# Kernel optimization log

Hardware: AMD Instinct MI355X
Metric: run time of the kernel (lower is better)

## Reference

```python
import jax, jax.numpy as jnp
import numpy as np

B = 65536
N_HOSTS = 16
N_FEATS = 48        # 3 * n_hosts
N_WINDOW = 3
N_LATENT = 10
GAT_IN = 3
GAT_OUT = 16
E = N_WINDOW + GAT_OUT  # 19, MHA embed dim
PROTO_DIM = 10


def setup_inputs() -> dict:
    key = jax.random.key(0)
    ks = jax.random.split(key, 20)
    def rn(k, shape, scale=0.1):
        return jax.random.normal(k, shape, dtype=jnp.float32) * scale
    return {
        "t": jax.random.normal(ks[0], (B, N_WINDOW, N_FEATS), dtype=jnp.float32),
        "s": jnp.zeros((1,), jnp.float32),  # unused by forward, kept for signature fidelity
        "h0": jax.random.normal(ks[1], (B, 1, N_WINDOW), dtype=jnp.float32),
        "gru_Wih": rn(ks[2], (3 * N_WINDOW, N_FEATS)),
        "gru_Whh": rn(ks[3], (3 * N_WINDOW, N_WINDOW)),
        "gru_bih": rn(ks[4], (3 * N_WINDOW,)),
        "gru_bhh": rn(ks[5], (3 * N_WINDOW,)),
        "gat_W": rn(ks[6], (GAT_IN, GAT_OUT)),
        "gat_al": rn(ks[7], (GAT_OUT,)),
        "gat_ar": rn(ks[8], (GAT_OUT,)),
        "mha_Win": rn(ks[9], (3 * E, E)),
        "mha_bin": rn(ks[10], (3 * E,)),
        "mha_Wout": rn(ks[11], (E, E)),
        "mha_bout": rn(ks[12], (E,)),
        "enc_W": rn(ks[13], (N_HOSTS * N_LATENT, N_WINDOW * E)),
        "enc_b": rn(ks[14], (N_HOSTS * N_LATENT,)),
        "anom_W": rn(ks[15], (2, N_LATENT)),
        "anom_b": rn(ks[16], (2,)),
        "proto_W": rn(ks[17], (PROTO_DIM, N_LATENT)),
        "proto_b": rn(ks[18], (PROTO_DIM,)),
    }


def _forward(t, s, h0, gru_Wih, gru_Whh, gru_bih, gru_bhh,
             gat_W, gat_al, gat_ar, mha_Win, mha_bin, mha_Wout, mha_bout,
             enc_W, enc_b, anom_W, anom_b, proto_W, proto_b):
    # ---- GRU (seq-first, batch B, hidden = n_window = 3) ----
    xs = jnp.swapaxes(t, 0, 1)  # (3, B, 48)
    h0_ = h0[:, 0, :]           # (B, 3)

    def gru_step(h, x_t):
        gi = x_t @ gru_Wih.T + gru_bih   # (B, 9)
        gh = h @ gru_Whh.T + gru_bhh     # (B, 9)
        i_r, i_z, i_n = jnp.split(gi, 3, axis=-1)
        h_r, h_z, h_n = jnp.split(gh, 3, axis=-1)
        r = jax.nn.sigmoid(i_r + h_r)
        z = jax.nn.sigmoid(i_z + h_z)
        n = jnp.tanh(i_n + r * h_n)
        h_new = (1.0 - z) * n + z * h
        return h_new, h_new

    _, gru_out = jax.lax.scan(gru_step, h0_, xs)  # (3, B, 3)

    # ---- GAT on fully-connected 16-node graph (with self loops) ----
    gin = t.reshape(t.shape[0], N_WINDOW, N_HOSTS, GAT_IN)      # (B, 3, 16, 3)
    z = jnp.einsum("bwnc,cf->bwnf", gin, gat_W)                 # (B, 3, 16, 16)
    el = z @ gat_al                                              # src scores (B,3,16)
    er = z @ gat_ar                                              # dst scores (B,3,16)
    e = jax.nn.leaky_relu(er[..., :, None] + el[..., None, :], 0.2)  # (B,3,v,u)
    alpha = jax.nn.softmax(e, axis=-1)                           # softmax over sources u
    gat_nodes = jnp.einsum("bwvu,bwuf->bwvf", alpha, z)          # (B, 3, 16, 16)
    gat_out = gat_nodes.mean(axis=2)                             # (B, 3, 16) mean over hosts
    gat_out = jnp.swapaxes(gat_out, 0, 1)                        # (3, B, 16)

    # ---- concat + single-head MHA (embed=19) ----
    c = jnp.concatenate([gru_out, gat_out], axis=-1)             # (3, B, 19)
    Wq, Wk, Wv = jnp.split(mha_Win, 3, axis=0)
    bq, bk, bv = jnp.split(mha_bin, 3, axis=0)
    q = c @ Wq.T + bq
    k = c @ Wk.T + bk
    v = c @ Wv.T + bv
    scores = jnp.einsum("sbe,tbe->bst", q, k) / jnp.sqrt(jnp.float32(E))
    attw = jax.nn.softmax(scores, axis=-1)
    attn = jnp.einsum("bst,tbe->sbe", attw, v)
    attn = attn @ mha_Wout.T + mha_bout                          # (3, B, 19)

    # ---- encoder: Linear(57,160); LeakyReLU(True) => negative_slope=1.0 => identity ----
    flat = jnp.swapaxes(attn, 0, 1).reshape(-1, N_WINDOW * E)    # (B, 57), seq-major flatten
    latent = flat @ enc_W.T + enc_b                              # (B, 160)
    latent = latent.reshape(-1, N_HOSTS, N_LATENT)               # (B, 16, 10)

    # ---- per-host tiny decoders, vectorized ----
    anomaly = jax.nn.softmax(latent @ anom_W.T + anom_b, axis=-1)   # (B, 16, 2)
    proto = jax.nn.sigmoid(latent @ proto_W.T + proto_b)            # (B, 16, PROTO_DIM)
    return anomaly, proto


def reference(t, s, h0, gru_Wih, gru_Whh, gru_bih, gru_bhh,
              gat_W, gat_al, gat_ar, mha_Win, mha_bin, mha_Wout, mha_bout,
              enc_W, enc_b, anom_W, anom_b, proto_W, proto_b):
    return _forward(t, s, h0, gru_Wih, gru_Whh, gru_bih, gru_bhh,
                    gat_W, gat_al, gat_ar, mha_Win, mha_bin, mha_Wout, mha_bout,
                    enc_W, enc_b, anom_W, anom_b, proto_W, proto_b)
```

## Files before the change

kernel.cpp:

```cpp
#include <hip/hip_runtime.h>

#define NW 3
#define NF 48
#define NHOST 16
#define NLAT 10
#define GOUT 16
#define EDIM 19
#define PDIM 10

#define CB_M    0
#define CB_P    361
#define CB_G    722
#define CB_H    741
#define CB_R    760
#define CB_C0   779
#define CB_WAL  780
#define CB_WAR  783
#define CB_CBIG 800
#define CB_BF   976
#define CB_TOT  10240

typedef __attribute__((ext_vector_type(8))) short bf16x8;
typedef __attribute__((ext_vector_type(4))) float f32x4;

__device__ __forceinline__ float frcp(float x){ return __builtin_amdgcn_rcpf(x); }
__device__ __forceinline__ float fsig(float x){ return frcp(1.f + __expf(-x)); }
__device__ __forceinline__ float ftanh(float x){ return 1.f - 2.f*frcp(1.f + __expf(2.f*x)); }
__device__ __forceinline__ unsigned short f2bf(float x){
    union { float f; unsigned u; } v; v.f = x;
    unsigned r = v.u + 0x7FFFu + ((v.u >> 16) & 1u);
    return (unsigned short)(r >> 16);
}

__global__ __launch_bounds__(256) void k_const(
    const float* __restrict__ Win, const float* __restrict__ bin,
    const float* __restrict__ Wout, const float* __restrict__ bout,
    const float* __restrict__ gatW, const float* __restrict__ gal,
    const float* __restrict__ gar, const float* __restrict__ encW,
    const float* __restrict__ encb,
    const float* __restrict__ aW, const float* __restrict__ ab,
    const float* __restrict__ pW, const float* __restrict__ pb,
    float* __restrict__ cb)
{
    const int w = blockIdx.x*blockDim.x + threadIdx.x;
    if (w < 786) {
        const int idx = w;
        float acc = 0.f;
        if (idx < 361) {
            int i = idx/19, j = idx%19;
            for (int e = 0; e < EDIM; ++e) acc += Win[e*EDIM+i]*Win[(EDIM+e)*EDIM+j];
        } else if (idx < 722) {
            int k = idx-361; int i = k/19, j = k%19;
            for (int e = 0; e < EDIM; ++e) acc += Wout[i*EDIM+e]*Win[(2*EDIM+e)*EDIM+j];
        } else if (idx < 741) {
            int j = idx-722;
            for (int e = 0; e < EDIM; ++e) acc += bin[e]*Win[(EDIM+e)*EDIM+j];
        } else if (idx < 760) {
            int i = idx-741;
            for (int e = 0; e < EDIM; ++e) acc += Win[e*EDIM+i]*bin[EDIM+e];
        } else if (idx < 779) {
            int i = idx-760; acc = bout[i];
            for (int e = 0; e < EDIM; ++e) acc += Wout[i*EDIM+e]*bin[2*EDIM+e];
        } else if (idx == 779) {
            for (int e = 0; e < EDIM; ++e) acc += bin[e]*bin[EDIM+e];
        } else {
            int c = idx-780; int cc = c%3; bool left = c<3;
            for (int f2 = 0; f2 < GOUT; ++f2)
                acc += gatW[cc*GOUT+f2]*(left ? gal[f2] : gar[f2]);
        }
        cb[idx] = acc;
    } else if (w < 962) {
        const int g = w - 786;
        int host = g / 11, jj = g % 11;
        float acc = (jj == 0) ? (ab[0] - ab[1]) : pb[jj-1];
        for (int l = 0; l < NLAT; ++l) {
            float coef = (jj == 0) ? (aW[l] - aW[NLAT+l]) : pW[(jj-1)*NLAT + l];
            acc += coef * encb[host*NLAT + l];
        }
        cb[CB_CBIG + g] = acc;
    } else if (w < 12226) {
        unsigned short* bf = (unsigned short*)(cb + CB_BF);
        const int u = w - 962;
        int j    = u & 7;
        int lane = (u >> 3) & 63;
        int tile = u >> 9;
        int half = tile / 11, n = tile % 11;
        int k = half*32 + ((lane >> 4) & 3)*8 + j;
        int g = n*16 + (lane & 15);
        float acc = 0.f;
        if (k < 57) {
            int host = g / 11, jj = g % 11;
            for (int l = 0; l < NLAT; ++l) {
                float coef = (jj == 0) ? (aW[l] - aW[NLAT+l]) : pW[(jj-1)*NLAT + l];
                acc += coef * encW[(host*NLAT + l)*57 + k];
            }
        }
        bf[u] = f2bf(acc);
    }
}

__global__ __launch_bounds__(256) void k_fused(
    const float* __restrict__ t, const float* __restrict__ h0,
    const float* __restrict__ Wih, const float* __restrict__ bih,
    const float* __restrict__ gatW, const float* __restrict__ Whh,
    const float* __restrict__ bhh, const float* __restrict__ cb,
    float* __restrict__ outA, float* __restrict__ outP, int B)
{
    __shared__ __align__(16) char smraw[57344];
    __shared__ __align__(16) unsigned short a2[64][64];
    float (*fm)[25][64] = reinterpret_cast<float(*)[25][64]>(smraw);
    float* xs            = reinterpret_cast<float*>(smraw + 19200);
    float (*mtb)[EDIM][64] = reinterpret_cast<float(*)[EDIM][64]>(smraw + 19200);
    float (*gtb)[64]       = reinterpret_cast<float(*)[64]>(smraw + 19200 + 14592);
    float (*pcb)[EDIM][64] = reinterpret_cast<float(*)[EDIM][64]>(smraw + 19200 + 15360);
    float (*lg)[178]       = reinterpret_cast<float(*)[178]>(smraw);

    const int tid = threadIdx.x;
    const int b0  = blockIdx.x * 64;
    const int bl  = tid & 63;
    const int sw  = tid >> 6;

    if (tid < 192) {
        const int w = sw;
        const float* tp = t + ((size_t)(b0 + bl)*NW + w)*NF;
        float* xrow = xs + tid*49;

        const float Wal0=cb[CB_WAL],Wal1=cb[CB_WAL+1],Wal2=cb[CB_WAL+2];
        const float War0=cb[CB_WAR],War1=cb[CB_WAR+1],War2=cb[CB_WAR+2];

        float gi[9];
#pragma unroll
        for (int r = 0; r < 9; ++r) gi[r] = bih[r];
        float el[NHOST], er[NHOST];
#pragma unroll
        for (int c = 0; c < 4; ++c) {
            float xc[12];
#pragma unroll
            for (int i = 0; i < 3; ++i) {
                float4 v = *reinterpret_cast<const float4*>(tp + c*12 + i*4);
                xc[i*4+0]=v.x; xc[i*4+1]=v.y; xc[i*4+2]=v.z; xc[i*4+3]=v.w;
            }
#pragma unroll
            for (int k = 0; k < 12; ++k) xrow[c*12 + k] = xc[k];
#pragma unroll
            for (int r = 0; r < 9; ++r) {
                float a = 0.f;
#pragma unroll
                for (int k = 0; k < 12; ++k) a += xc[k]*Wih[r*NF + c*12 + k];
                gi[r] += a;
            }
#pragma unroll
            for (int u = 0; u < 4; ++u) {
                const int uu = c*4 + u;
                el[uu] = xc[u*3]*Wal0 + xc[u*3+1]*Wal1 + xc[u*3+2]*Wal2;
                er[uu] = xc[u*3]*War0 + xc[u*3+1]*War1 + xc[u*3+2]*War2;
            }
        }
#pragma unroll
        for (int r = 0; r < 9; ++r) fm[w][r][bl] = gi[r];

        float beta[NHOST];
#pragma unroll
        for (int u = 0; u < NHOST; ++u) beta[u] = 0.f;
#pragma unroll
        for (int v = 0; v < NHOST; ++v) {
            float ee[NHOST]; float sum = 0.f;
#pragma unroll
            for (int u = 0; u < NHOST; ++u) {
                float s = er[v] + el[u];
                s = fmaxf(s, 0.2f*s);
                ee[u] = __expf(s); sum += ee[u];
            }
            float inv = frcp(sum);
#pragma unroll
            for (int u = 0; u < NHOST; ++u) beta[u] += ee[u]*inv;
        }
        float g0=0.f, g1=0.f, g2=0.f;
#pragma unroll
        for (int u = 0; u < NHOST; ++u) {
            float bu = beta[u]*(1.f/16.f);
            g0 += bu*xrow[u*3+0]; g1 += bu*xrow[u*3+1]; g2 += bu*xrow[u*3+2];
        }
#pragma unroll
        for (int f2 = 0; f2 < GOUT; ++f2)
            fm[w][9+f2][bl] = g0*gatW[f2] + g1*gatW[GOUT+f2] + g2*gatW[2*GOUT+f2];
    }
    __syncthreads();

    float cw[EDIM];
    float hsv = 0.f, aw0 = 0.f, aw1 = 0.f, aw2 = 0.f;
#pragma unroll
    for (int i = 0; i < EDIM; ++i) cw[i] = 0.f;

    if (tid < 192) {
        const int s = sw;
        const int b = b0 + bl;
        float h[3] = { h0[(size_t)b*3+0], h0[(size_t)b*3+1], h0[(size_t)b*3+2] };
        float ch[NW][3];
#pragma unroll
        for (int w = 0; w < NW; ++w) {
            float gi[9];
#pragma unroll
            for (int r = 0; r < 9; ++r) gi[r] = fm[w][r][bl];
            float gh[9];
#pragma unroll
            for (int r = 0; r < 9; ++r)
                gh[r] = bhh[r] + h[0]*Whh[r*3+0] + h[1]*Whh[r*3+1] + h[2]*Whh[r*3+2];
#pragma unroll
            for (int j = 0; j < 3; ++j) {
                float rg = fsig(gi[j]   + gh[j]);
                float zg = fsig(gi[3+j] + gh[3+j]);
                float ng = ftanh(gi[6+j] + rg*gh[6+j]);
                h[j] = (1.f - zg)*ng + zg*h[j];
            }
            ch[w][0]=h[0]; ch[w][1]=h[1]; ch[w][2]=h[2];
        }
#pragma unroll
        for (int j = 0; j < 3; ++j)
            cw[j] = (s==0) ? ch[0][j] : (s==1) ? ch[1][j] : ch[2][j];
#pragma unroll
        for (int f2 = 0; f2 < GOUT; ++f2)
            cw[3+f2] = fm[s][9+f2][bl];

        float gt = 0.f;
#pragma unroll
        for (int i = 0; i < EDIM; ++i) { hsv += cw[i]*cb[CB_H+i]; gt += cw[i]*cb[CB_G+i]; }
#pragma unroll
        for (int i = 0; i < EDIM; ++i) {
            float a = 0.f;
#pragma unroll
            for (int j = 0; j < EDIM; ++j) a += cb[CB_M+i*EDIM+j]*cw[j];
            mtb[s][i][bl] = a;
        }
        gtb[s][bl] = gt;
    }
    __syncthreads();

    if (tid < 192) {
        const int s = sw;
        const float c0 = cb[CB_C0];
        float sc[NW];
#pragma unroll
        for (int tt = 0; tt < NW; ++tt) {
            float a = 0.f;
#pragma unroll
            for (int i = 0; i < EDIM; ++i) a += cw[i]*mtb[tt][i][bl];
            sc[tt] = (a + gtb[tt][bl] + hsv + c0) * 0.2294157338705618f;
        }
        float m = fmaxf(sc[0], fmaxf(sc[1], sc[2]));
        float e0=__expf(sc[0]-m), e1=__expf(sc[1]-m), e2=__expf(sc[2]-m);
        float inv = frcp(e0+e1+e2);
        aw0=e0*inv; aw1=e1*inv; aw2=e2*inv;

#pragma unroll
        for (int i = 0; i < EDIM; ++i) {
            float a = 0.f;
#pragma unroll
            for (int j = 0; j < EDIM; ++j) a += cb[CB_P+i*EDIM+j]*cw[j];
            pcb[s][i][bl] = a;
        }
    }
    __syncthreads();

    if (tid < 192) {
        const int s = sw;
        char* a2c = (char*)a2;
        const int swz = (bl & 7) << 4;
#pragma unroll
        for (int i = 0; i < EDIM; ++i) {
            float v = cb[CB_R+i] + aw0*pcb[0][i][bl] + aw1*pcb[1][i][bl]
                    + aw2*pcb[2][i][bl];
            const int byte = bl*128 + (s*EDIM + i)*2;
            *reinterpret_cast<unsigned short*>(a2c + (byte ^ swz)) = f2bf(v);
        }
        if (s == 0) {
#pragma unroll
            for (int r = 0; r < 7; ++r) {
                const int byte = bl*128 + (57 + r)*2;
                *reinterpret_cast<unsigned short*>(a2c + (byte ^ swz)) = 0;
            }
        }
    }
    __syncthreads();

    const int lane = tid & 63;
    const int wv   = __builtin_amdgcn_readfirstlane(sw);
    {
        const int browl = wv*16 + (lane & 15);
        const int koff  = (lane >> 4) * 8;
        const char* a2c = (const char*)a2;
        const int swz = (browl & 7) << 4;
        union { uint4 q; bf16x8 v; } a0, a1;
        a0.q = *reinterpret_cast<const uint4*>(a2c + ((browl*128 + koff*2) ^ swz));
        a1.q = *reinterpret_cast<const uint4*>(a2c + ((browl*128 + 64 + koff*2) ^ swz));

        const uint4* bfq = (const uint4*)(cb + CB_BF);
        const int r0 = wv*16 + ((lane >> 4) << 2);
#pragma unroll
        for (int n = 0; n < 11; ++n) {
            union { uint4 q; bf16x8 v; } bf0, bf1;
            bf0.q = bfq[(size_t)n*64 + lane];
            bf1.q = bfq[(size_t)(11 + n)*64 + lane];
            f32x4 acc = {0.f, 0.f, 0.f, 0.f};
            acc = __builtin_amdgcn_mfma_f32_16x16x32_bf16(a0.v, bf0.v, acc, 0, 0, 0);
            acc = __builtin_amdgcn_mfma_f32_16x16x32_bf16(a1.v, bf1.v, acc, 0, 0, 0);
            const int c = n*16 + (lane & 15);
#pragma unroll
            for (int r = 0; r < 4; ++r) lg[r0 + r][c] = acc[r];
        }
    }
    __syncthreads();

    {
        const int host = tid & 15;
        const int tg   = tid >> 4;
        const float* cbig = cb + CB_CBIG;
#pragma unroll
        for (int i = 0; i < 4; ++i) {
            const int bll = tg + 16*i;
            const int b   = b0 + bll;
            float v[11];
#pragma unroll
            for (int jj = 0; jj < 11; ++jj)
                v[jj] = lg[bll][host*11 + jj] + cbig[host*11 + jj];
            float p0 = fsig(v[0]);
            float2 av; av.x = p0; av.y = 1.f - p0;
            *reinterpret_cast<float2*>(outA + (size_t)b*32 + host*2) = av;
            float* pP = outP + (size_t)b*160 + host*10;
#pragma unroll
            for (int p = 0; p < 5; ++p) {
                float2 pv; pv.x = fsig(v[1 + 2*p]); pv.y = fsig(v[2 + 2*p]);
                *reinterpret_cast<float2*>(pP + 2*p) = pv;
            }
        }
    }
}

extern "C" void kernel_launch(void* const* d_in, const int* in_sizes, int n_in,
                              void* d_out, int out_size, void* d_ws, size_t ws_size,
                              hipStream_t stream) {
    const float* t    = (const float*)d_in[0];
    const float* h0   = (const float*)d_in[2];
    const float* Wih  = (const float*)d_in[3];
    const float* Whh  = (const float*)d_in[4];
    const float* bih  = (const float*)d_in[5];
    const float* bhh  = (const float*)d_in[6];
    const float* gatW = (const float*)d_in[7];
    const float* gal  = (const float*)d_in[8];
    const float* gar  = (const float*)d_in[9];
    const float* Win  = (const float*)d_in[10];
    const float* bin  = (const float*)d_in[11];
    const float* Wout = (const float*)d_in[12];
    const float* bout = (const float*)d_in[13];
    const float* encW = (const float*)d_in[14];
    const float* encb = (const float*)d_in[15];
    const float* aW   = (const float*)d_in[16];
    const float* ab   = (const float*)d_in[17];
    const float* pW   = (const float*)d_in[18];
    const float* pb   = (const float*)d_in[19];

    const int B = in_sizes[0] / (NW * NF);
    float* cb  = (float*)d_ws;
    float* outA = (float*)d_out;
    float* outP = (float*)d_out + (size_t)B*32;

    k_const<<<dim3(48), 256, 0, stream>>>(Win, bin, Wout, bout, gatW, gal, gar,
                                          encW, encb, aW, ab, pW, pb, cb);
    k_fused<<<dim3(B/64), 256, 0, stream>>>(t, h0, Wih, bih, gatW, Whh, bhh, cb,
                                            outA, outP, B);
}
```

Baseline: 64.97 us.

## Shrink fused kernel to single-wave blocks of 16 rows with compact LDS

Changes the fused kernel from 256-thread blocks over 64 batch rows to 64-thread single-wavefront blocks over 16 rows. It cuts LDS per block by storing the input rows as bf16 and the MFMA logits as fp16, and adds extra barriers so that aliased shared buffers are not overwritten early. The aim is higher occupancy and more blocks in flight, at the cost of 48 of 64 lanes working in the early stages, four times as many blocks, and lower precision in the intermediates.

Result: no change. 66.18 us (+1.9%).

```diff
diff --git a/kernel.cpp b/kernel.cpp
--- a/kernel.cpp
+++ b/kernel.cpp
@@ -30,6 +30,9 @@
     union { float f; unsigned u; } v; v.f = x;
     unsigned r = v.u + 0x7FFFu + ((v.u >> 16) & 1u);
     return (unsigned short)(r >> 16);
+}
+__device__ __forceinline__ float bf2f(unsigned short s){
+    union { unsigned u; float f; } v; v.u = ((unsigned)s) << 16; return v.f;
 }
 
 __global__ __launch_bounds__(256) void k_const(
@@ -99,31 +102,31 @@
     }
 }
 
-__global__ __launch_bounds__(256) void k_fused(
+__global__ __launch_bounds__(64, 4) void k_fused(
     const float* __restrict__ t, const float* __restrict__ h0,
     const float* __restrict__ Wih, const float* __restrict__ bih,
     const float* __restrict__ gatW, const float* __restrict__ Whh,
     const float* __restrict__ bhh, const float* __restrict__ cb,
     float* __restrict__ outA, float* __restrict__ outP, int B)
 {
-    __shared__ __align__(16) char smraw[57344];
-    __shared__ __align__(16) unsigned short a2[64][64];
-    float (*fm)[25][64] = reinterpret_cast<float(*)[25][64]>(smraw);
-    float* xs            = reinterpret_cast<float*>(smraw + 19200);
-    float (*mtb)[EDIM][64] = reinterpret_cast<float(*)[EDIM][64]>(smraw + 19200);
-    float (*gtb)[64]       = reinterpret_cast<float(*)[64]>(smraw + 19200 + 14592);
-    float (*pcb)[EDIM][64] = reinterpret_cast<float(*)[EDIM][64]>(smraw + 19200 + 15360);
-    float (*lg)[178]       = reinterpret_cast<float(*)[178]>(smraw);
-
-    const int tid = threadIdx.x;
-    const int b0  = blockIdx.x * 64;
-    const int bl  = tid & 63;
-    const int sw  = tid >> 6;
-
-    if (tid < 192) {
+    __shared__ __align__(16) char smraw[9600];
+    __shared__ __align__(16) unsigned short a2[16][64];
+    float (*fm)[25][16]     = reinterpret_cast<float(*)[25][16]>(smraw);
+    unsigned short (*xs)[50]= reinterpret_cast<unsigned short(*)[50]>(smraw + 4800);
+    float (*mtb)[EDIM][16]  = reinterpret_cast<float(*)[EDIM][16]>(smraw + 4800);
+    float (*pcb)[EDIM][16]  = reinterpret_cast<float(*)[EDIM][16]>(smraw + 4800);
+    float (*gtb)[16]        = reinterpret_cast<float(*)[16]>(smraw + 4800 + 3648);
+    _Float16 (*lg)[178]     = reinterpret_cast<_Float16(*)[178]>(smraw);
+
+    const int lane = threadIdx.x;
+    const int b0   = blockIdx.x * 16;
+    const int bl   = lane & 15;
+    const int sw   = lane >> 4;
+
+    if (lane < 48) {
         const int w = sw;
         const float* tp = t + ((size_t)(b0 + bl)*NW + w)*NF;
-        float* xrow = xs + tid*49;
+        unsigned short* xrow = xs[lane];
 
         const float Wal0=cb[CB_WAL],Wal1=cb[CB_WAL+1],Wal2=cb[CB_WAL+2];
         const float War0=cb[CB_WAR],War1=cb[CB_WAR+1],War2=cb[CB_WAR+2];
@@ -141,7 +144,7 @@
                 xc[i*4+0]=v.x; xc[i*4+1]=v.y; xc[i*4+2]=v.z; xc[i*4+3]=v.w;
             }
 #pragma unroll
-            for (int k = 0; k < 12; ++k) xrow[c*12 + k] = xc[k];
+            for (int k = 0; k < 12; ++k) xrow[c*12 + k] = f2bf(xc[k]);
 #pragma unroll
             for (int r = 0; r < 9; ++r) {
                 float a = 0.f;
@@ -179,7 +182,9 @@
 #pragma unroll
         for (int u = 0; u < NHOST; ++u) {
             float bu = beta[u]*(1.f/16.f);
-            g0 += bu*xrow[u*3+0]; g1 += bu*xrow[u*3+1]; g2 += bu*xrow[u*3+2];
+            g0 += bu*bf2f(xrow[u*3+0]);
+            g1 += bu*bf2f(xrow[u*3+1]);
+            g2 += bu*bf2f(xrow[u*3+2]);
         }
 #pragma unroll
         for (int f2 = 0; f2 < GOUT; ++f2)
@@ -192,7 +197,7 @@
 #pragma unroll
     for (int i = 0; i < EDIM; ++i) cw[i] = 0.f;
 
-    if (tid < 192) {
+    if (lane < 48) {
         const int s = sw;
         const int b = b0 + bl;
         float h[3] = { h0[(size_t)b*3+0], h0[(size_t)b*3+1], h0[(size_t)b*3+2] };
@@ -221,7 +226,11 @@
 #pragma unroll
         for (int f2 = 0; f2 < GOUT; ++f2)
             cw[3+f2] = fm[s][9+f2][bl];
-
+    }
+    __syncthreads();
+
+    if (lane < 48) {
+        const int s = sw;
         float gt = 0.f;
 #pragma unroll
         for (int i = 0; i < EDIM; ++i) { hsv += cw[i]*cb[CB_H+i]; gt += cw[i]*cb[CB_G+i]; }
@@ -236,8 +245,7 @@
     }
     __syncthreads();
 
-    if (tid < 192) {
-        const int s = sw;
+    if (lane < 48) {
         const float c0 = cb[CB_C0];
         float sc[NW];
 #pragma unroll
@@ -251,7 +259,11 @@
         float e0=__expf(sc[0]-m), e1=__expf(sc[1]-m), e2=__expf(sc[2]-m);
         float inv = frcp(e0+e1+e2);
         aw0=e0*inv; aw1=e1*inv; aw2=e2*inv;
-
+    }
+    __syncthreads();
+
+    if (lane < 48) {
+        const int s = sw;
 #pragma unroll
         for (int i = 0; i < EDIM; ++i) {
             float a = 0.f;
@@ -262,7 +274,7 @@
     }
     __syncthreads();
 
-    if (tid < 192) {
+    if (lane < 48) {
         const int s = sw;
         char* a2c = (char*)a2;
         const int swz = (bl & 7) << 4;
@@ -283,10 +295,8 @@
     }
     __syncthreads();
 
-    const int lane = tid & 63;
-    const int wv   = __builtin_amdgcn_readfirstlane(sw);
     {
-        const int browl = wv*16 + (lane & 15);
+        const int browl = lane & 15;
         const int koff  = (lane >> 4) * 8;
         const char* a2c = (const char*)a2;
         const int swz = (browl & 7) << 4;
@@ -295,7 +305,7 @@
         a1.q = *reinterpret_cast<const uint4*>(a2c + ((browl*128 + 64 + koff*2) ^ swz));
 
         const uint4* bfq = (const uint4*)(cb + CB_BF);
-        const int r0 = wv*16 + ((lane >> 4) << 2);
+        const int r0 = (lane >> 4) << 2;
 #pragma unroll
         for (int n = 0; n < 11; ++n) {
             union { uint4 q; bf16x8 v; } bf0, bf1;
@@ -306,23 +316,23 @@
             acc = __builtin_amdgcn_mfma_f32_16x16x32_bf16(a1.v, bf1.v, acc, 0, 0, 0);
             const int c = n*16 + (lane & 15);
 #pragma unroll
-            for (int r = 0; r < 4; ++r) lg[r0 + r][c] = acc[r];
+            for (int r = 0; r < 4; ++r) lg[r0 + r][c] = (_Float16)acc[r];
         }
     }
     __syncthreads();
 
     {
-        const int host = tid & 15;
-        const int tg   = tid >> 4;
+        const int host = lane & 15;
+        const int tg   = lane >> 4;
         const float* cbig = cb + CB_CBIG;
 #pragma unroll
         for (int i = 0; i < 4; ++i) {
-            const int bll = tg + 16*i;
+            const int bll = tg + 4*i;
             const int b   = b0 + bll;
             float v[11];
 #pragma unroll
             for (int jj = 0; jj < 11; ++jj)
-                v[jj] = lg[bll][host*11 + jj] + cbig[host*11 + jj];
+                v[jj] = (float)lg[bll][host*11 + jj] + cbig[host*11 + jj];
             float p0 = fsig(v[0]);
             float2 av; av.x = p0; av.y = 1.f - p0;
             *reinterpret_cast<float2*>(outA + (size_t)b*32 + host*2) = av;
@@ -366,6 +376,6 @@
 
     k_const<<<dim3(48), 256, 0, stream>>>(Win, bin, Wout, bout, gatW, gal, gar,
                                           encW, encb, aW, ab, pW, pb, cb);
-    k_fused<<<dim3(B/64), 256, 0, stream>>>(t, h0, Wih, bih, gatW, Whh, bhh, cb,
-                                            outA, outP, B);
-}
+    k_fused<<<dim3(B/16), 64, 0, stream>>>(t, h0, Wih, bih, gatW, Whh, bhh, cb,
+                                           outA, outP, B);
+}
```
